# Optimization experiments

Measured on AMD Instinct MI355X. Metric: run time of the kernel, lower is better.

## Reference

```python
import jax, jax.numpy as jnp
import numpy as np

N_FEAT = 256
B, T = 8, 2048


def setup_inputs() -> dict:
    key = jax.random.key(0)
    k1, k2, k3, k4, k5, k6 = jax.random.split(key, 6)
    feat = jax.random.normal(k1, (B, T, N_FEAT), dtype=jnp.float32)
    hlens = jax.random.randint(k2, (B,), 1, T + 1, dtype=jnp.int32)
    # torch nn.Linear params: weight [out, in], bias [out]
    lim = 1.0 / np.sqrt(N_FEAT)
    Wq = jax.random.uniform(k3, (N_FEAT, N_FEAT), jnp.float32, -lim, lim)
    bq = jax.random.uniform(k4, (N_FEAT,), jnp.float32, -lim, lim)
    Wk = jax.random.uniform(k5, (N_FEAT, N_FEAT), jnp.float32, -lim, lim)
    bk = jax.random.uniform(k6, (N_FEAT,), jnp.float32, -lim, lim)
    return {"feat": feat, "hlens": hlens, "Wq": Wq, "bq": bq, "Wk": Wk, "bk": bk}


def reference(feat, hlens, Wq, bq, Wk, bk):
    # q/k projections (torch Linear: x @ W^T + b)
    q = jnp.einsum('btf,gf->btg', feat, Wq) + bq  # [B, T, F]
    k = jnp.einsum('btf,gf->btg', feat, Wk) + bk  # [B, T, F]
    sa = jnp.einsum('btf,bsf->bts', q, k)         # [B, T, T] full score matrix
    score = jnp.mean(sa, axis=-1)                 # [B, T]
    attn = jax.nn.softmax(sa, axis=-1)            # [B, T, T]
    feat_new = jnp.einsum('bts,bsf->btf', attn, feat)  # [B, T, F]
    # peaks is overwritten to all-True in the original, so hlens_new = T and
    # the per-batch gather loop is an identity copy -> feat_new unchanged.
    hlens_new = jnp.full((feat.shape[0],), feat.shape[1], dtype=jnp.int32)
    return feat_new, hlens_new, score
```

## Files before the change

kernel.cpp:

```cpp
#include <hip/hip_runtime.h>
#include <math.h>

#define B_ 8
#define T_ 2048
#define F_ 256
#define M_TOT (B_ * T_)

typedef __attribute__((ext_vector_type(8))) short short8;
typedef __attribute__((ext_vector_type(4))) float floatx4;

__device__ __forceinline__ short f2bf(float x) {
    unsigned u = __float_as_uint(x);
    u += 0x7FFF + ((u >> 16) & 1);
    return (short)(u >> 16);
}
__device__ __forceinline__ float bf2f(short s) {
    return __uint_as_float(((unsigned)(unsigned short)s) << 16);
}

__device__ __forceinline__ void cp_g2l_16(const void* g, void* l) {
    __builtin_amdgcn_global_load_lds(
        (const __attribute__((address_space(1))) void*)g,
        (__attribute__((address_space(3))) void*)l, 16, 0, 0);
}

__global__ __launch_bounds__(256) void pack_feat_all(
    const float* __restrict__ feat,
    short* __restrict__ featAh, short* __restrict__ featAl,
    short* __restrict__ stg, float* __restrict__ featpart)
{
    __shared__ float lds[32][260];
    const int tid = threadIdx.x;
    const int kc  = blockIdx.x;
    const int b   = blockIdx.y;

#pragma unroll
    for (int i = 0; i < 8; ++i) {
        const int lin = i * 256 + tid;
        const int r = lin >> 6, c4 = (lin & 63) * 4;
        float4 v = *(const float4*)&feat[((size_t)b * T_ + kc * 32 + r) * F_ + c4];
        lds[r][c4 + 0] = v.x; lds[r][c4 + 1] = v.y;
        lds[r][c4 + 2] = v.z; lds[r][c4 + 3] = v.w;
    }
    __syncthreads();

    const int lane = tid & 63, w = tid >> 6;
    const int quad = lane >> 4, l15 = lane & 15;

#pragma unroll
    for (int i = 0; i < 4; ++i) {
        const int idx = w * 4 + i;
        const int r16h = idx >> 3, fc = idx & 7;
        float v[8];
        *(float4*)&v[0] = *(const float4*)&lds[r16h * 16 + l15][fc * 32 + quad * 8];
        *(float4*)&v[4] = *(const float4*)&lds[r16h * 16 + l15][fc * 32 + quad * 8 + 4];
        short8 h, l;
#pragma unroll
        for (int j = 0; j < 8; ++j) {
            const short hh = f2bf(v[j]);
            h[j] = hh; l[j] = f2bf(v[j] - bf2f(hh));
        }
        const int r16 = b * 128 + kc * 2 + r16h;
        const size_t dst = ((size_t)r16 * 8 + fc) * 512 + lane * 8;
        *(short8*)&featAh[dst] = h;
        *(short8*)&featAl[dst] = l;
    }

#pragma unroll
    for (int fi = 0; fi < 4; ++fi) {
        const int ft = w + fi * 4;
        short8 h;
#pragma unroll
        for (int j = 0; j < 8; ++j)
            h[j] = f2bf(lds[quad * 8 + j][ft * 16 + l15]);
        const size_t dst = ((size_t)(b * 64 + kc)) * 16384 + 8192 + ft * 512 + lane * 8;
        *(short8*)&stg[dst] = h;
    }

    {
        float s = 0.f;
#pragma unroll
        for (int r = 0; r < 32; ++r) s += lds[r][tid];
        featpart[((size_t)b * 64 + kc) * 256 + tid] = s;
    }
}

__global__ __launch_bounds__(256) void pack_w(
    const float* __restrict__ Wq, const float* __restrict__ Wk,
    short* __restrict__ wfqh, short* __restrict__ wfql,
    short* __restrict__ wfkh)
{
    const int tid = threadIdx.x, lane = tid & 63, w = tid >> 6;
    const int idx = blockIdx.x * 4 + w;
    const int isk = idx >> 7, nt = (idx >> 3) & 15, fc = idx & 7;
    const int quad = lane >> 4, l15 = lane & 15;
    const float* __restrict__ W = isk ? Wk : Wq;
    const int row = nt * 16 + l15, col = fc * 32 + quad * 8;

    float v[8];
    *(float4*)&v[0] = *(const float4*)&W[(size_t)row * F_ + col];
    *(float4*)&v[4] = *(const float4*)&W[(size_t)row * F_ + col + 4];
    const size_t dst = ((size_t)(nt * 8 + fc)) * 512 + lane * 8;
    if (isk) {
        short8 h;
#pragma unroll
        for (int j = 0; j < 8; ++j) h[j] = f2bf(v[j]);
        *(short8*)&wfkh[dst] = h;
    } else {
        short8 h, l;
#pragma unroll
        for (int j = 0; j < 8; ++j) {
            const short hh = f2bf(v[j]);
            h[j] = hh; l[j] = f2bf(v[j] - bf2f(hh));
        }
        *(short8*)&wfqh[dst] = h;
        *(short8*)&wfql[dst] = l;
    }
}

__global__ __launch_bounds__(256) void wvec_kernel(
    const float* __restrict__ featpart,
    const float* __restrict__ Wq, const float* __restrict__ bq,
    const float* __restrict__ Wk, const float* __restrict__ bk,
    float* __restrict__ wv, float* __restrict__ cv,
    float* __restrict__ out_hlens)
{
    __shared__ float fb[256];
    __shared__ float kb[256];
    const int b = blockIdx.x, tid = threadIdx.x;

    float s = 0.f;
#pragma unroll 8
    for (int c = 0; c < 64; ++c) s += featpart[((size_t)b * 64 + c) * 256 + tid];
    fb[tid] = s * (1.0f / (float)T_);
    __syncthreads();

    float acc = bk[tid];
#pragma unroll 8
    for (int f = 0; f < 256; ++f) acc += Wk[(size_t)tid * 256 + f] * fb[f];
    kb[tid] = acc;
    __syncthreads();

    float wf_ = 0.f;
#pragma unroll 8
    for (int g = 0; g < 256; ++g) wf_ += Wq[(size_t)g * 256 + tid] * kb[g];
    wv[b * 256 + tid] = wf_;

    __syncthreads();
    fb[tid] = bq[tid] * kb[tid];
    __syncthreads();
    for (int st = 128; st > 0; st >>= 1) {
        if (tid < st) fb[tid] += fb[tid + st];
        __syncthreads();
    }
    if (tid == 0) cv[b] = fb[0];
    if (b == 0 && tid < B_) out_hlens[tid] = (float)T_;
}

__global__ __launch_bounds__(256) void score_kernel(
    const float* __restrict__ feat, const float* __restrict__ wv,
    const float* __restrict__ cv, float* __restrict__ out_score)
{
    __shared__ float wl[256];
    const int tid = threadIdx.x;
    const int b   = blockIdx.x >> 5;
    const int t0s = (blockIdx.x & 31) * 64;
    wl[tid] = wv[b * 256 + tid];
    __syncthreads();

    const int row = t0s + (tid >> 2);
    const int fq  = (tid & 3) * 64;
    const float* fr = &feat[((size_t)b * T_ + row) * F_ + fq];
    float s = 0.f;
#pragma unroll
    for (int i = 0; i < 16; ++i) {
        float4 v = *(const float4*)&fr[i * 4];
        s += v.x * wl[fq + i * 4 + 0] + v.y * wl[fq + i * 4 + 1]
           + v.z * wl[fq + i * 4 + 2] + v.w * wl[fq + i * 4 + 3];
    }
    s += __shfl_xor(s, 1, 64);
    s += __shfl_xor(s, 2, 64);
    if ((tid & 3) == 0) out_score[(size_t)b * T_ + row] = s + cv[b];
}

__global__ __launch_bounds__(512, 4) void proj_mfma(
    const short* __restrict__ featAh, const short* __restrict__ featAl,
    const short* __restrict__ wfqh, const short* __restrict__ wfql,
    const short* __restrict__ wfkh,
    const float* __restrict__ bq, const float* __restrict__ bk,
    short* __restrict__ qfh, short* __restrict__ qfl,
    short* __restrict__ stg)
{
    __shared__ short wbuf[2][8192];
    __shared__ float Tr[8][16][36];

    const int tid = threadIdx.x, lane = tid & 63, w = tid >> 6;
    const int quad = lane >> 4, l15 = lane & 15;
    const int x  = blockIdx.x;
    const int ng = x & 3, rg = x >> 2;
    const bool isq = ng < 2;
    const int r16 = rg * 8 + w;
    const int b = r16 >> 7, qt16 = r16 & 127;
    const int ntb = isq ? ng * 8 : (ng - 2) * 8;

    short8 ah[8], al[8];
#pragma unroll
    for (int fc = 0; fc < 8; ++fc) {
        const size_t off = ((size_t)r16 * 8 + fc) * 512 + lane * 8;
        ah[fc] = *(const short8*)&featAh[off];
        al[fc] = *(const short8*)&featAl[off];
    }

    const short* __restrict__ wsh = (isq ? wfqh : wfkh) + (size_t)ntb * 4096;
    const short* __restrict__ wsl = wfql + (size_t)ntb * 4096;
    const float* __restrict__ bias = isq ? bq : bk;

    cp_g2l_16(wsh + tid * 8, &wbuf[0][tid * 8]);
    if (isq) cp_g2l_16(wsl + tid * 8, &wbuf[0][4096 + tid * 8]);

    int cur = 0;
    for (int i = 0; i < 8; ++i, cur ^= 1) {
        __syncthreads();

        floatx4 C = (floatx4){0.f, 0.f, 0.f, 0.f};
#pragma unroll
        for (int fc = 0; fc < 8; ++fc) {
            short8 wh = *(const short8*)&wbuf[cur][fc * 512 + lane * 8];
            C = __builtin_amdgcn_mfma_f32_16x16x32_bf16(ah[fc], wh, C, 0, 0, 0);
            C = __builtin_amdgcn_mfma_f32_16x16x32_bf16(al[fc], wh, C, 0, 0, 0);
            if (isq) {
                short8 wl2 = *(const short8*)&wbuf[cur][4096 + fc * 512 + lane * 8];
                C = __builtin_amdgcn_mfma_f32_16x16x32_bf16(ah[fc], wl2, C, 0, 0, 0);
            }
        }

        if (i + 1 < 8) {
            cp_g2l_16(wsh + (size_t)(i + 1) * 4096 + tid * 8,
                      &wbuf[cur ^ 1][tid * 8]);
            if (isq) cp_g2l_16(wsl + (size_t)(i + 1) * 4096 + tid * 8,
                               &wbuf[cur ^ 1][4096 + tid * 8]);
        }

        const int nt = ntb + i;
        const float bv = bias[nt * 16 + l15];
        const int ch = (i & 1) * 16;
#pragma unroll
        for (int r = 0; r < 4; ++r)
            Tr[w][quad * 4 + r][ch + l15] = C[r] + bv;

        if (i & 1) {
            float v[8];
            *(float4*)&v[0] = *(const float4*)&Tr[w][l15][quad * 8];
            *(float4*)&v[4] = *(const float4*)&Tr[w][l15][quad * 8 + 4];
            const int p = nt >> 1;
            if (isq) {
                short8 h, l;
#pragma unroll
                for (int j = 0; j < 8; ++j) {
                    const short hh = f2bf(v[j]);
                    h[j] = hh; l[j] = f2bf(v[j] - bf2f(hh));
                }
                const size_t dst = ((size_t)(b * 8 + p) * 128 + qt16) * 512 + lane * 8;
                *(short8*)&qfh[dst] = h;
                *(short8*)&qfl[dst] = l;
            } else {
                short8 h;
#pragma unroll
                for (int j = 0; j < 8; ++j) h[j] = f2bf(v[j]);
                const size_t dst = ((size_t)(b * 64 + (qt16 >> 1))) * 16384
                                 + (p * 2 + (qt16 & 1)) * 512 + lane * 8;
                *(short8*)&stg[dst] = h;
            }
        }
    }
}

__global__ __launch_bounds__(256, 2) void attn_mfma(
    const short* __restrict__ qfh_g, const short* __restrict__ qfl_g,
    const short* __restrict__ stg,
    float* __restrict__ o0, float* __restrict__ o1,
    float* __restrict__ lpart)
{
    __shared__ short kbuf[2][16384];
    __shared__ float P_lds[64 * 36];
    __shared__ float l_lds[2][64];

    const int tid  = threadIdx.x;
    const int wave = tid >> 6, lane = tid & 63;
    const int qp   = wave & 1, fh = wave >> 1;
    const int quad = lane >> 4, l15 = lane & 15;

    const int lid  = blockIdx.x;
    const int b    = lid & 7;
    const int qt   = (lid >> 3) & 31;
    const int ks   = lid >> 8;

    short8 qh[2][8], ql[2][8];
#pragma unroll
    for (int t = 0; t < 2; ++t) {
        const int qt16 = qt * 4 + qp * 2 + t;
#pragma unroll
        for (int fc = 0; fc < 8; ++fc) {
            const size_t off = ((size_t)(b * 8 + fc) * 128 + qt16) * 512 + lane * 8;
            qh[t][fc] = *(const short8*)&qfh_g[off];
            ql[t][fc] = *(const short8*)&qfl_g[off];
        }
    }

    floatx4 O[2][8];
#pragma unroll
    for (int t = 0; t < 2; ++t)
#pragma unroll
        for (int i = 0; i < 8; ++i) O[t][i] = (floatx4){0.f, 0.f, 0.f, 0.f};
    float lsum[2][4] = {};

    const short* sbase = &stg[(size_t)b * 64 * 16384];
    const int kbeg = ks * 32, kend = kbeg + 32;

    {
        const short* src = sbase + (size_t)kbeg * 16384 + tid * 8;
        short* dst = &kbuf[0][tid * 8];
#pragma unroll
        for (int i = 0; i < 8; ++i)
            cp_g2l_16(src + i * 2048, dst + i * 2048);
    }

    int cur = 0;
    for (int kt = kbeg; kt < kend; ++kt, cur ^= 1) {
        __syncthreads();

        floatx4 Sa[2], Sb[2];
#pragma unroll
        for (int t = 0; t < 2; ++t) {
            Sa[t] = (floatx4){0.f, 0.f, 0.f, 0.f};
            Sb[t] = (floatx4){0.f, 0.f, 0.f, 0.f};
        }
#pragma unroll
        for (int fc = 0; fc < 8; ++fc) {
            short8 bh = *(const short8*)&kbuf[cur][(fc * 2 + fh) * 512 + lane * 8];
#pragma unroll
            for (int t = 0; t < 2; ++t) {
                Sa[t] = __builtin_amdgcn_mfma_f32_16x16x32_bf16(qh[t][fc], bh, Sa[t], 0, 0, 0);
                Sb[t] = __builtin_amdgcn_mfma_f32_16x16x32_bf16(ql[t][fc], bh, Sb[t], 0, 0, 0);
            }
        }

#pragma unroll
        for (int t = 0; t < 2; ++t)
#pragma unroll
            for (int r = 0; r < 4; ++r) {
                const float e = __expf(Sa[t][r] + Sb[t][r]);
                lsum[t][r] += e;
                P_lds[((qp * 2 + t) * 16 + quad * 4 + r) * 36 + fh * 16 + l15] = e;
            }
        __syncthreads();

        short8 ph[2], pl[2];
#pragma unroll
        for (int t = 0; t < 2; ++t) {
            float pv[8];
            *(float4*)&pv[0] = *(const float4*)&P_lds[((qp * 2 + t) * 16 + l15) * 36 + quad * 8];
            *(float4*)&pv[4] = *(const float4*)&P_lds[((qp * 2 + t) * 16 + l15) * 36 + quad * 8 + 4];
#pragma unroll
            for (int j = 0; j < 8; ++j) {
                const short hh = f2bf(pv[j]);
                ph[t][j] = hh;
                pl[t][j] = f2bf(pv[j] - bf2f(hh));
            }
        }

        if (kt + 1 < kend) {
            const short* src = sbase + (size_t)(kt + 1) * 16384 + tid * 8;
            short* dst = &kbuf[cur ^ 1][tid * 8];
#pragma unroll
            for (int i = 0; i < 8; ++i)
                cp_g2l_16(src + i * 2048, dst + i * 2048);
        }

#pragma unroll
        for (int ft = 0; ft < 8; ++ft) {
            short8 fv = *(const short8*)&kbuf[cur][8192 + (fh * 8 + ft) * 512 + lane * 8];
#pragma unroll
            for (int t = 0; t < 2; ++t) {
                O[t][ft] = __builtin_amdgcn_mfma_f32_16x16x32_bf16(ph[t], fv, O[t][ft], 0, 0, 0);
                O[t][ft] = __builtin_amdgcn_mfma_f32_16x16x32_bf16(pl[t], fv, O[t][ft], 0, 0, 0);
            }
        }
    }

#pragma unroll
    for (int t = 0; t < 2; ++t)
#pragma unroll
        for (int r = 0; r < 4; ++r) {
            lsum[t][r] += __shfl_xor(lsum[t][r], 1, 64);
            lsum[t][r] += __shfl_xor(lsum[t][r], 2, 64);
            lsum[t][r] += __shfl_xor(lsum[t][r], 4, 64);
            lsum[t][r] += __shfl_xor(lsum[t][r], 8, 64);
        }
    if (l15 == 0) {
#pragma unroll
        for (int t = 0; t < 2; ++t)
#pragma unroll
            for (int r = 0; r < 4; ++r)
                l_lds[fh][(qp * 2 + t) * 16 + quad * 4 + r] = lsum[t][r];
    }
    __syncthreads();

    float* __restrict__ opart = ks ? o1 : o0;
    const size_t row0 = (size_t)b * T_ + qt * 64;

    if (tid < 64)
        __builtin_nontemporal_store(l_lds[0][tid] + l_lds[1][tid],
                                    &lpart[(size_t)ks * M_TOT + row0 + tid]);

#pragma unroll
    for (int t = 0; t < 2; ++t)
#pragma unroll
        for (int r = 0; r < 4; ++r) {
            const int qr = (qp * 2 + t) * 16 + quad * 4 + r;
#pragma unroll
            for (int ft = 0; ft < 8; ++ft)
                __builtin_nontemporal_store(
                    O[t][ft][r],
                    &opart[(row0 + qr) * F_ + fh * 128 + ft * 16 + l15]);
        }
}

__global__ __launch_bounds__(256) void combine_kernel(
    float* __restrict__ out_feat, const float* __restrict__ o1,
    const float* __restrict__ lpart)
{
    const size_t gid = (size_t)blockIdx.x * 256 + threadIdx.x;
    const size_t row = gid >> 6;
    const float inv = 1.0f / (lpart[row] + lpart[M_TOT + row]);
    floatx4 a  = __builtin_nontemporal_load(&((const floatx4*)out_feat)[gid]);
    floatx4 bx = __builtin_nontemporal_load(&((const floatx4*)o1)[gid]);
    a = (a + bx) * inv;
    __builtin_nontemporal_store(a, &((floatx4*)out_feat)[gid]);
}

extern "C" void kernel_launch(void* const* d_in, const int* in_sizes, int n_in,
                              void* d_out, int out_size, void* d_ws, size_t ws_size,
                              hipStream_t stream)
{
    const float* feat = (const float*)d_in[0];
    const float* Wq = (const float*)d_in[2];
    const float* bq = (const float*)d_in[3];
    const float* Wk = (const float*)d_in[4];
    const float* bk = (const float*)d_in[5];

    float* out_feat  = (float*)d_out;
    float* out_hlens = out_feat + (size_t)M_TOT * F_;
    float* out_score = out_hlens + B_;

    short* featAh = (short*)d_ws;
    short* featAl = featAh + (size_t)M_TOT * F_;
    short* qfh    = featAl + (size_t)M_TOT * F_;
    short* qfl    = qfh + (size_t)M_TOT * F_;
    short* stg    = qfl + (size_t)M_TOT * F_;
    short* wfqh   = stg + (size_t)2 * M_TOT * F_;
    short* wfql   = wfqh + 65536;
    short* wfkh   = wfql + 65536;
    float* featpart = (float*)(wfkh + 65536);
    float* wv     = featpart + 131072;
    float* cv     = wv + 2048;
    float* o1     = (float*)featAh;
    float* lpart  = featpart;

    dim3 fgrid(64, B_);
    pack_feat_all<<<fgrid, 256, 0, stream>>>(feat, featAh, featAl, stg, featpart);

    pack_w<<<64, 256, 0, stream>>>(Wq, Wk, wfqh, wfql, wfkh);

    wvec_kernel<<<B_, 256, 0, stream>>>(featpart, Wq, bq, Wk, bk, wv, cv, out_hlens);

    score_kernel<<<256, 256, 0, stream>>>(feat, wv, cv, out_score);

    proj_mfma<<<512, 512, 0, stream>>>(featAh, featAl, wfqh, wfql, wfkh,
                                       bq, bk, qfh, qfl, stg);

    attn_mfma<<<512, 256, 0, stream>>>(qfh, qfl, stg, out_feat, o1, lpart);

    combine_kernel<<<M_TOT * F_ / 4 / 256, 256, 0, stream>>>(out_feat, o1, lpart);
}
```

Baseline: 209.0 us.

## Drop low-order P split in PV MFMA, fuse weight packing, use nontemporal stores

The attention PV product now uses only the bf16-high part of the softmax probabilities, which halves the PV MFMA count and removes the hi/lo split arithmetic. Weight packing is folded into pack_feat_all as an extra block column, saving one kernel launch. Stores of packed feat and q fragments become nontemporal to reduce cache pollution. The cost is lower precision in the attention output, since P is rounded to plain bf16.

```diff
diff --git a/kernel.cpp b/kernel.cpp
--- a/kernel.cpp
+++ b/kernel.cpp
@@ -27,10 +27,46 @@
 __global__ __launch_bounds__(256) void pack_feat_all(
     const float* __restrict__ feat,
     short* __restrict__ featAh, short* __restrict__ featAl,
-    short* __restrict__ stg, float* __restrict__ featpart)
-{
+    short* __restrict__ stg, float* __restrict__ featpart,
+    const float* __restrict__ Wq, const float* __restrict__ Wk,
+    short* __restrict__ wfqh, short* __restrict__ wfql,
+    short* __restrict__ wfkh)
+{
+    const int tid = threadIdx.x;
+    const int lane = tid & 63, w = tid >> 6;
+    const int quad = lane >> 4, l15 = lane & 15;
+
+    if (blockIdx.x == 64) {
+#pragma unroll
+        for (int i = 0; i < 8; ++i) {
+            const int idx = blockIdx.y * 32 + w * 8 + i;
+            const int isk = idx >> 7, nt = (idx >> 3) & 15, fc = idx & 7;
+            const float* __restrict__ W = isk ? Wk : Wq;
+            const int row = nt * 16 + l15, col = fc * 32 + quad * 8;
+            float v[8];
+            *(float4*)&v[0] = *(const float4*)&W[(size_t)row * F_ + col];
+            *(float4*)&v[4] = *(const float4*)&W[(size_t)row * F_ + col + 4];
+            const size_t dst = ((size_t)(nt * 8 + fc)) * 512 + lane * 8;
+            if (isk) {
+                short8 h;
+#pragma unroll
+                for (int j = 0; j < 8; ++j) h[j] = f2bf(v[j]);
+                *(short8*)&wfkh[dst] = h;
+            } else {
+                short8 h, l;
+#pragma unroll
+                for (int j = 0; j < 8; ++j) {
+                    const short hh = f2bf(v[j]);
+                    h[j] = hh; l[j] = f2bf(v[j] - bf2f(hh));
+                }
+                *(short8*)&wfqh[dst] = h;
+                *(short8*)&wfql[dst] = l;
+            }
+        }
+        return;
+    }
+
     __shared__ float lds[32][260];
-    const int tid = threadIdx.x;
     const int kc  = blockIdx.x;
     const int b   = blockIdx.y;
 
@@ -43,9 +79,6 @@
         lds[r][c4 + 2] = v.z; lds[r][c4 + 3] = v.w;
     }
     __syncthreads();
-
-    const int lane = tid & 63, w = tid >> 6;
-    const int quad = lane >> 4, l15 = lane & 15;
 
 #pragma unroll
     for (int i = 0; i < 4; ++i) {
@@ -62,8 +95,8 @@
         }
         const int r16 = b * 128 + kc * 2 + r16h;
         const size_t dst = ((size_t)r16 * 8 + fc) * 512 + lane * 8;
-        *(short8*)&featAh[dst] = h;
-        *(short8*)&featAl[dst] = l;
+        __builtin_nontemporal_store(h, (short8*)&featAh[dst]);
+        __builtin_nontemporal_store(l, (short8*)&featAl[dst]);
     }
 
 #pragma unroll
@@ -82,39 +115,6 @@
 #pragma unroll
         for (int r = 0; r < 32; ++r) s += lds[r][tid];
         featpart[((size_t)b * 64 + kc) * 256 + tid] = s;
-    }
-}
-
-__global__ __launch_bounds__(256) void pack_w(
-    const float* __restrict__ Wq, const float* __restrict__ Wk,
-    short* __restrict__ wfqh, short* __restrict__ wfql,
-    short* __restrict__ wfkh)
-{
-    const int tid = threadIdx.x, lane = tid & 63, w = tid >> 6;
-    const int idx = blockIdx.x * 4 + w;
-    const int isk = idx >> 7, nt = (idx >> 3) & 15, fc = idx & 7;
-    const int quad = lane >> 4, l15 = lane & 15;
-    const float* __restrict__ W = isk ? Wk : Wq;
-    const int row = nt * 16 + l15, col = fc * 32 + quad * 8;
-
-    float v[8];
-    *(float4*)&v[0] = *(const float4*)&W[(size_t)row * F_ + col];
-    *(float4*)&v[4] = *(const float4*)&W[(size_t)row * F_ + col + 4];
-    const size_t dst = ((size_t)(nt * 8 + fc)) * 512 + lane * 8;
-    if (isk) {
-        short8 h;
-#pragma unroll
-        for (int j = 0; j < 8; ++j) h[j] = f2bf(v[j]);
-        *(short8*)&wfkh[dst] = h;
-    } else {
-        short8 h, l;
-#pragma unroll
-        for (int j = 0; j < 8; ++j) {
-            const short hh = f2bf(v[j]);
-            h[j] = hh; l[j] = f2bf(v[j] - bf2f(hh));
-        }
-        *(short8*)&wfqh[dst] = h;
-        *(short8*)&wfql[dst] = l;
     }
 }
 
@@ -261,8 +261,8 @@
                     h[j] = hh; l[j] = f2bf(v[j] - bf2f(hh));
                 }
                 const size_t dst = ((size_t)(b * 8 + p) * 128 + qt16) * 512 + lane * 8;
-                *(short8*)&qfh[dst] = h;
-                *(short8*)&qfl[dst] = l;
+                __builtin_nontemporal_store(h, (short8*)&qfh[dst]);
+                __builtin_nontemporal_store(l, (short8*)&qfl[dst]);
             } else {
                 short8 h;
 #pragma unroll
@@ -355,18 +355,15 @@
             }
         __syncthreads();
 
-        short8 ph[2], pl[2];
+        short8 ph[2];
 #pragma unroll
         for (int t = 0; t < 2; ++t) {
             float pv[8];
             *(float4*)&pv[0] = *(const float4*)&P_lds[((qp * 2 + t) * 16 + l15) * 36 + quad * 8];
             *(float4*)&pv[4] = *(const float4*)&P_lds[((qp * 2 + t) * 16 + l15) * 36 + quad * 8 + 4];
 #pragma unroll
-            for (int j = 0; j < 8; ++j) {
-                const short hh = f2bf(pv[j]);
-                ph[t][j] = hh;
-                pl[t][j] = f2bf(pv[j] - bf2f(hh));
-            }
+            for (int j = 0; j < 8; ++j)
+                ph[t][j] = f2bf(pv[j]);
         }
 
         if (kt + 1 < kend) {
@@ -381,10 +378,8 @@
         for (int ft = 0; ft < 8; ++ft) {
             short8 fv = *(const short8*)&kbuf[cur][8192 + (fh * 8 + ft) * 512 + lane * 8];
 #pragma unroll
-            for (int t = 0; t < 2; ++t) {
+            for (int t = 0; t < 2; ++t)
                 O[t][ft] = __builtin_amdgcn_mfma_f32_16x16x32_bf16(ph[t], fv, O[t][ft], 0, 0, 0);
-                O[t][ft] = __builtin_amdgcn_mfma_f32_16x16x32_bf16(pl[t], fv, O[t][ft], 0, 0, 0);
-            }
         }
     }
 
@@ -467,10 +462,9 @@
     float* o1     = (float*)featAh;
     float* lpart  = featpart;
 
-    dim3 fgrid(64, B_);
-    pack_feat_all<<<fgrid, 256, 0, stream>>>(feat, featAh, featAl, stg, featpart);
-
-    pack_w<<<64, 256, 0, stream>>>(Wq, Wk, wfqh, wfql, wfkh);
+    dim3 fgrid(65, B_);
+    pack_feat_all<<<fgrid, 256, 0, stream>>>(feat, featAh, featAl, stg, featpart,
+                                             Wq, Wk, wfqh, wfql, wfkh);
 
     wvec_kernel<<<B_, 256, 0, stream>>>(featpart, Wq, bq, Wk, bk, wv, cv, out_hlens);
 
```

Measured after the change: 192.9 us. -7.7%, faster.
